# Kernel optimization log

Measured on AMD Instinct MI355X. Metric: run time of the kernel, lower is better.

The kernel has to match this reference:

```python
import math
import jax, jax.numpy as jnp
import numpy as np

GRID = 512
BATCH = 4


def _grid_faces(g: int) -> np.ndarray:
    # Standard two-triangles-per-quad triangulation of a g x g vertex grid.
    idx = np.arange(g * g, dtype=np.int32).reshape(g, g)
    v00 = idx[:-1, :-1].ravel()
    v01 = idx[:-1, 1:].ravel()
    v10 = idx[1:, :-1].ravel()
    v11 = idx[1:, 1:].ravel()
    f1 = np.stack([v00, v10, v01], axis=1)
    f2 = np.stack([v01, v10, v11], axis=1)
    return np.concatenate([f1, f2], axis=0)  # [2*(g-1)^2, 3]


def setup_inputs() -> dict:
    key = jax.random.key(0)
    n_verts = GRID * GRID
    X = jax.random.normal(key, (BATCH, 3, n_verts), dtype=jnp.float32)
    faces = jnp.asarray(_grid_faces(GRID), dtype=jnp.int32)
    return {"X": X, "faces": faces}


def reference(X, faces):
    B, _, N = X.shape
    g = int(math.isqrt(N))
    V = jnp.transpose(X, (0, 2, 1))  # [B, N, 3] vertices

    v0, v1, v2 = faces[:, 0], faces[:, 1], faces[:, 2]
    e0 = V[:, v1, :] - V[:, v0, :]  # [B, F, 3]
    e1 = V[:, v2, :] - V[:, v0, :]
    e2 = V[:, v1, :] - V[:, v2, :]

    def _unit(e):
        return e / jnp.sqrt(jnp.sum(e * e, axis=2, keepdims=True))

    e0n, e1n, e2n = _unit(e0), _unit(e1), _unit(e2)

    a0 = jnp.arccos(jnp.sum(e0n * e1n, axis=2))  # [B, F]
    a1 = jnp.arccos(jnp.sum(e2n * e0n, axis=2))
    a2 = math.pi - (a1 - a0)

    tn = jnp.cross(e0, e2, axis=2)  # [B, F, 3] triangle normals

    # Sequential scatter-set, matching torch overwrite semantics (v2 last).
    normals = jnp.zeros_like(V)
    normals = normals.at[:, v0, :].set(tn * a0[..., None])
    normals = normals.at[:, v1, :].set(tn * a1[..., None])
    normals = normals.at[:, v2, :].set(tn * a2[..., None])

    visibility = (normals[:, :, 2] >= 0)  # [B, N] bool
    mask = visibility.reshape(B, g, g).astype(X.dtype)
    # repeat_interleave(mask, 3, 0).reshape(B,3,g,g) == broadcast over channel dim
    mask4 = jnp.broadcast_to(mask[:, None, :, :], (B, 3, g, g))
    return 1.0 - mask4
```

## Files before the change

kernel.cpp:

```cpp
#include <hip/hip_runtime.h>
#include <math.h>


#define G     512
#define NV    (G * G)
#define BATCH 4

__global__ __launch_bounds__(256) void vis_mask_kernel(const float* __restrict__ X,
                                                       float* __restrict__ out) {
    int tid = blockIdx.x * blockDim.x + threadIdx.x;
    if (tid >= BATCH * NV) return;

    int b = tid >> 18;
    int v = tid & (NV - 1);
    int R = v >> 9;
    int C = v & (G - 1);

    int r0, c0, r1, c1, r2, c2, aidx;
    if (R >= 1 && C >= 1)      { r0 = R - 1; c0 = C;     r1 = R; c1 = C - 1; r2 = R; c2 = C; aidx = 2; }
    else if (R == 0 && C >= 1) { r0 = 0;     c0 = C - 1; r1 = 1; c1 = C - 1; r2 = 0; c2 = C; aidx = 2; }
    else if (C == 0 && R >= 1) { r0 = R - 1; c0 = 1;     r1 = R; c1 = 0;     r2 = R; c2 = 1; aidx = 1; }
    else                       { r0 = 0;     c0 = 0;     r1 = 1; c1 = 0;     r2 = 0; c2 = 1; aidx = 0; }

    const float* Xb = X + (size_t)b * 3 * NV;
    int i0 = r0 * G + c0;
    int i1 = r1 * G + c1;
    int i2 = r2 * G + c2;

    float v0x = Xb[i0],          v0y = Xb[NV + i0],      v0z = Xb[2 * NV + i0];
    float v1x = Xb[i1],          v1y = Xb[NV + i1],      v1z = Xb[2 * NV + i1];
    float v2x = Xb[i2],          v2y = Xb[NV + i2],      v2z = Xb[2 * NV + i2];

    float e0x = v1x - v0x, e0y = v1y - v0y, e0z = v1z - v0z;
    float e1x = v2x - v0x, e1y = v2y - v0y, e1z = v2z - v0z;
    float e2x = v1x - v2x, e2y = v1y - v2y, e2z = v1z - v2z;

    float n0 = sqrtf(e0x * e0x + e0y * e0y + e0z * e0z);
    float n1 = sqrtf(e1x * e1x + e1y * e1y + e1z * e1z);
    float n2 = sqrtf(e2x * e2x + e2y * e2y + e2z * e2z);

    float e0nx = e0x / n0, e0ny = e0y / n0, e0nz = e0z / n0;
    float e1nx = e1x / n1, e1ny = e1y / n1, e1nz = e1z / n1;
    float e2nx = e2x / n2, e2ny = e2y / n2, e2nz = e2z / n2;

    float a0 = acosf(e0nx * e1nx + e0ny * e1ny + e0nz * e1nz);
    float a1 = acosf(e2nx * e0nx + e2ny * e0ny + e2nz * e0nz);
    float a2 = (float)M_PI - (a1 - a0);

    float angle = (aidx == 2) ? a2 : ((aidx == 1) ? a1 : a0);

    float tnz  = __fsub_rn(__fmul_rn(e0x, e2y), __fmul_rn(e0y, e2x));
    float prod = __fmul_rn(tnz, angle);

    float o = (prod >= 0.0f) ? 0.0f : 1.0f;

    size_t base = ((size_t)b * 3) * NV + (size_t)v;
    out[base]          = o;
    out[base + NV]     = o;
    out[base + 2 * NV] = o;
}

extern "C" void kernel_launch(void* const* d_in, const int* in_sizes, int n_in,
                              void* d_out, int out_size, void* d_ws, size_t ws_size,
                              hipStream_t stream) {
    const float* X = (const float*)d_in[0];
    float* out = (float*)d_out;

    int total = BATCH * NV;
    int block = 256;
    int grid  = (total + block - 1) / block;
    vis_mask_kernel<<<grid, block, 0, stream>>>(X, out);
}
```

Measured before the change: 73.94 us.

## Process four vertices per thread with float4 loads and stores

Each thread now handles four adjacent columns of a row. It loads the current row and the neighbour row as float4 vectors per coordinate plane, plus one scalar halo element, and reuses those registers across the four vertex computations. The three output planes are written as float4 stores. This cuts the number of load instructions and redundant neighbour fetches and widens memory transactions, in exchange for more registers per thread and a quarter as many threads.

```diff
diff --git a/kernel.cpp b/kernel.cpp
--- a/kernel.cpp
+++ b/kernel.cpp
@@ -6,31 +6,10 @@
 #define NV    (G * G)
 #define BATCH 4
 
-__global__ __launch_bounds__(256) void vis_mask_kernel(const float* __restrict__ X,
-                                                       float* __restrict__ out) {
-    int tid = blockIdx.x * blockDim.x + threadIdx.x;
-    if (tid >= BATCH * NV) return;
-
-    int b = tid >> 18;
-    int v = tid & (NV - 1);
-    int R = v >> 9;
-    int C = v & (G - 1);
-
-    int r0, c0, r1, c1, r2, c2, aidx;
-    if (R >= 1 && C >= 1)      { r0 = R - 1; c0 = C;     r1 = R; c1 = C - 1; r2 = R; c2 = C; aidx = 2; }
-    else if (R == 0 && C >= 1) { r0 = 0;     c0 = C - 1; r1 = 1; c1 = C - 1; r2 = 0; c2 = C; aidx = 2; }
-    else if (C == 0 && R >= 1) { r0 = R - 1; c0 = 1;     r1 = R; c1 = 0;     r2 = R; c2 = 1; aidx = 1; }
-    else                       { r0 = 0;     c0 = 0;     r1 = 1; c1 = 0;     r2 = 0; c2 = 1; aidx = 0; }
-
-    const float* Xb = X + (size_t)b * 3 * NV;
-    int i0 = r0 * G + c0;
-    int i1 = r1 * G + c1;
-    int i2 = r2 * G + c2;
-
-    float v0x = Xb[i0],          v0y = Xb[NV + i0],      v0z = Xb[2 * NV + i0];
-    float v1x = Xb[i1],          v1y = Xb[NV + i1],      v1z = Xb[2 * NV + i1];
-    float v2x = Xb[i2],          v2y = Xb[NV + i2],      v2z = Xb[2 * NV + i2];
-
+__device__ __forceinline__ float vis_o(float v0x, float v0y, float v0z,
+                                       float v1x, float v1y, float v1z,
+                                       float v2x, float v2y, float v2z,
+                                       int aidx) {
     float e0x = v1x - v0x, e0y = v1y - v0y, e0z = v1z - v0z;
     float e1x = v2x - v0x, e1y = v2y - v0y, e1z = v2z - v0z;
     float e2x = v1x - v2x, e2y = v1y - v2y, e2z = v1z - v2z;
@@ -51,13 +30,68 @@
 
     float tnz  = __fsub_rn(__fmul_rn(e0x, e2y), __fmul_rn(e0y, e2x));
     float prod = __fmul_rn(tnz, angle);
+    return (prod >= 0.0f) ? 0.0f : 1.0f;
+}
 
-    float o = (prod >= 0.0f) ? 0.0f : 1.0f;
+__global__ __launch_bounds__(256) void vis_mask_kernel(const float* __restrict__ X,
+                                                       float* __restrict__ out) {
+    int tid = blockIdx.x * blockDim.x + threadIdx.x;
+    int b  = tid >> 16;
+    int t  = tid & 65535;
+    int R  = t >> 7;
+    int Cg = t & 127;
+    int C  = Cg << 2;
 
-    size_t base = ((size_t)b * 3) * NV + (size_t)v;
-    out[base]          = o;
-    out[base + NV]     = o;
-    out[base + 2 * NV] = o;
+    const float* Xb = X + (size_t)b * 3 * NV;
+    int rB = (R >= 1) ? (R - 1) : 1;
+
+    float A[3][5], Bv[3][5];
+    #pragma unroll
+    for (int p = 0; p < 3; ++p) {
+        const float* plane = Xb + p * NV;
+        float4 a4 = *reinterpret_cast<const float4*>(plane + R  * G + C);
+        float4 b4 = *reinterpret_cast<const float4*>(plane + rB * G + C);
+        A[p][1] = a4.x; A[p][2] = a4.y; A[p][3] = a4.z; A[p][4] = a4.w;
+        Bv[p][1] = b4.x; Bv[p][2] = b4.y; Bv[p][3] = b4.z; Bv[p][4] = b4.w;
+        A[p][0] = 0.0f; Bv[p][0] = 0.0f;
+        if (C > 0) {
+            A[p][0] = plane[R * G + C - 1];
+            if (R == 0) Bv[p][0] = plane[rB * G + C - 1];
+        }
+    }
+
+    float o[4];
+    #pragma unroll
+    for (int j = 0; j < 4; ++j) {
+        int c = C + j;
+        if (R >= 1) {
+            if (c >= 1) {
+                o[j] = vis_o(Bv[0][j + 1], Bv[1][j + 1], Bv[2][j + 1],
+                             A[0][j],      A[1][j],      A[2][j],
+                             A[0][j + 1],  A[1][j + 1],  A[2][j + 1], 2);
+            } else {
+                o[j] = vis_o(Bv[0][2], Bv[1][2], Bv[2][2],
+                             A[0][1],  A[1][1],  A[2][1],
+                             A[0][2],  A[1][2],  A[2][2], 1);
+            }
+        } else {
+            if (c >= 1) {
+                o[j] = vis_o(A[0][j],     A[1][j],     A[2][j],
+                             Bv[0][j],    Bv[1][j],    Bv[2][j],
+                             A[0][j + 1], A[1][j + 1], A[2][j + 1], 2);
+            } else {
+                o[j] = vis_o(A[0][1],  A[1][1],  A[2][1],
+                             Bv[0][1], Bv[1][1], Bv[2][1],
+                             A[0][2],  A[1][2],  A[2][2], 0);
+            }
+        }
+    }
+
+    float4 ov = make_float4(o[0], o[1], o[2], o[3]);
+    size_t base = ((size_t)b * 3) * NV + (size_t)(R * G + C);
+    *reinterpret_cast<float4*>(out + base)          = ov;
+    *reinterpret_cast<float4*>(out + base + NV)     = ov;
+    *reinterpret_cast<float4*>(out + base + 2 * NV) = ov;
 }
 
 extern "C" void kernel_launch(void* const* d_in, const int* in_sizes, int n_in,
@@ -66,7 +100,7 @@
     const float* X = (const float*)d_in[0];
     float* out = (float*)d_out;
 
-    int total = BATCH * NV;
+    int total = BATCH * (NV / 4);
     int block = 256;
     int grid  = (total + block - 1) / block;
     vis_mask_kernel<<<grid, block, 0, stream>>>(X, out);
```

Result: slower. 76.60 us (+3.6%).
